# Performance work log

Measured on AMD Instinct MI355X. Metric: run time of the kernel, lower is better.

## Reference

```python
import jax, jax.numpy as jnp
import numpy as np

DIM = 1024
N_HEADS = 16
D_K = DIM // N_HEADS
B, N = 2, 2048


def _pairwise_dist(p):
    # p: [B, N, 3] -> Euclidean cdist [B, N, N], grad-safe at zero distance
    sq = jnp.sum(p * p, axis=-1)                      # [B, N]
    d2 = sq[:, :, None] + sq[:, None, :] - 2.0 * jnp.einsum('bnd,bmd->bnm', p, p)
    d2 = jnp.maximum(d2, 0.0)
    safe = jnp.where(d2 > 0.0, d2, 1.0)
    return jnp.where(d2 > 0.0, jnp.sqrt(safe), 0.0)


def setup_inputs() -> dict:
    key = jax.random.key(0)
    ks = jax.random.split(key, 11)
    s = 1.0 / np.sqrt(DIM)
    inp = {
        'x': jax.random.normal(ks[0], (B, N, DIM), jnp.float32),
        'positions': jax.random.normal(ks[1], (B, N, 3), jnp.float32),
        'W_q': jax.random.normal(ks[2], (DIM, DIM), jnp.float32) * s,
        'b_q': jnp.zeros((DIM,), jnp.float32),
        'W_k': jax.random.normal(ks[3], (DIM, DIM), jnp.float32) * s,
        'b_k': jnp.zeros((DIM,), jnp.float32),
        'W_v': jax.random.normal(ks[4], (DIM, DIM), jnp.float32) * s,
        'b_v': jnp.zeros((DIM,), jnp.float32),
        'W_o': jax.random.normal(ks[5], (DIM, DIM), jnp.float32) * s,
        'b_o': jnp.zeros((DIM,), jnp.float32),
        'dist_bias': jax.random.normal(ks[6], (N_HEADS, 1, 1), jnp.float32),
    }
    return inp


def reference(x, positions, W_q, b_q, W_k, b_k, W_v, b_v, W_o, b_o, dist_bias):
    Bv, Nv, C = x.shape
    def proj(W, b):
        # [B,N,C] -> [B,H,N,d_k]
        return (x @ W.T + b).reshape(Bv, Nv, N_HEADS, D_K).transpose(0, 2, 1, 3)
    Q = proj(W_q, b_q)
    K = proj(W_k, b_k)
    V = proj(W_v, b_v)
    attn = jnp.einsum('bhnd,bhmd->bhnm', Q, K) / np.sqrt(D_K)  # [B,H,N,N]
    dists = _pairwise_dist(positions)                          # [B,N,N]
    # log(exp(-|b|*d) + 1e-8), per-head bias broadcast over [B,H,N,N]
    dist_weights = jnp.exp(-jnp.abs(dist_bias)[None] * dists[:, None])
    attn = attn + jnp.log(dist_weights + 1e-8)
    attn = jax.nn.softmax(attn, axis=-1)
    out = jnp.einsum('bhnm,bhmd->bhnd', attn, V)               # [B,H,N,d_k]
    out = out.transpose(0, 2, 1, 3).reshape(Bv, Nv, C)
    return out @ W_o.T + b_o
```

## Files before the change

kernel.cpp:

```cpp
#include <hip/hip_runtime.h>
#include <hip/hip_bf16.h>
#include <stdint.h>

using bf16   = __hip_bfloat16;
using short8 = __attribute__((ext_vector_type(8))) short;
using f32x4  = __attribute__((ext_vector_type(4))) float;
using f32x16 = __attribute__((ext_vector_type(16))) float;

#define NSEQ   2048
#define NHEADS 16
#define DK     64
#define DMODEL 1024

#define GLDS16(gp, lp) __builtin_amdgcn_global_load_lds( \
    (const __attribute__((address_space(1))) void*)(gp), \
    (__attribute__((address_space(3))) void*)(lp), 16, 0, 0)

__device__ __forceinline__ ushort f2bf(float f){
  bf16 h = __float2bfloat16(f);
  return __builtin_bit_cast(ushort, h);
}
__device__ __forceinline__ float bf2f(ushort u){
  uint t = ((uint)u)<<16; return __builtin_bit_cast(float, t);
}

__global__ void k_cvt(const float4* __restrict__ src, ushort4* __restrict__ dst, int n4){
  int i = blockIdx.x*blockDim.x + threadIdx.x;
  if (i >= n4) return;
  float4 v = src[i];
  ushort4 o;
  o.x = f2bf(v.x); o.y = f2bf(v.y); o.z = f2bf(v.z); o.w = f2bf(v.w);
  dst[i] = o;
}

__global__ void k_geo(const float* __restrict__ pos, ushort* __restrict__ AF,
                      ushort* __restrict__ BF, int n){
  int i = blockIdx.x*blockDim.x + threadIdx.x;
  if (i >= n) return;
  float x = pos[i*3+0], y = pos[i*3+1], z = pos[i*3+2];
  float sq = x*x + y*y + z*z;
  ushort xh = f2bf(x);  float xhf = bf2f(xh);  ushort xl = f2bf(x - xhf);
  ushort yh = f2bf(y);  float yhf = bf2f(yh);  ushort yl = f2bf(y - yhf);
  ushort zh = f2bf(z);  float zhf = bf2f(zh);  ushort zl = f2bf(z - zhf);
  ushort sh = f2bf(sq); float shf = bf2f(sh);  ushort sl = f2bf(sq - shf);
  ushort m2xh = f2bf(-2.f*xhf), m2xl = f2bf(-2.f*bf2f(xl));
  ushort m2yh = f2bf(-2.f*yhf), m2yl = f2bf(-2.f*bf2f(yl));
  ushort m2zh = f2bf(-2.f*zhf), m2zl = f2bf(-2.f*bf2f(zl));
  const ushort one = 0x3F80;
  ushort af[16] = {xh,xl,xh, yh,yl,yh, zh,zl,zh, sh,sl, one,one, 0,0,0};
  ushort bv[16] = {m2xh,m2xh,m2xl, m2yh,m2yh,m2yl, m2zh,m2zh,m2zl, one,one, sh,sl, 0,0,0};
  *(uint4*)&AF[i*16]     = *(uint4*)&af[0];
  *(uint4*)&AF[i*16 + 8] = *(uint4*)&af[8];
  *(uint4*)&BF[i*16]     = *(uint4*)&bv[0];
  *(uint4*)&BF[i*16 + 8] = *(uint4*)&bv[8];
}

__device__ __forceinline__ void gemm_core(
    const ushort* __restrict__ Ap, const ushort* __restrict__ Bp,
    int bm, int bn, int tid, ushort smem[2][2][4096], f32x4 (&acc)[4][4])
{
  const int wave = tid>>6, lane = tid&63;
  const int wr = wave>>1, wc = wave&1;
  const int ko   = (lane>>4)*8;
  const int srow = wave*16 + (lane>>2);
  const int scol = (lane&3)*8;

  const ushort* As = Ap + (size_t)(bm*128)*DMODEL + scol;
  const ushort* Bs = Bp + (size_t)(bn*128)*DMODEL + scol;

#define STAGEG(buf, kt) do { \
    _Pragma("unroll") \
    for (int i_=0;i_<2;i_++){ \
      GLDS16(As + (size_t)(i_*64 + srow)*DMODEL + (kt)*32, &smem[buf][0][i_*2048 + wave*512]); \
      GLDS16(Bs + (size_t)(i_*64 + srow)*DMODEL + (kt)*32, &smem[buf][1][i_*2048 + wave*512]); \
    } } while(0)

  STAGEG(0, 0);
  for (int kt=0; kt<32; ++kt){
    int cur = kt&1;
    __syncthreads();
    if (kt<31) STAGEG(cur^1, kt+1);
    short8 af[4], bfv[4];
    const ushort* At = smem[cur][0];
    const ushort* Bt = smem[cur][1];
    #pragma unroll
    for (int mi=0;mi<4;mi++) af[mi]  = *(const short8*)&At[(wr*64+mi*16+(lane&15))*32 + ko];
    #pragma unroll
    for (int ni=0;ni<4;ni++) bfv[ni] = *(const short8*)&Bt[(wc*64+ni*16+(lane&15))*32 + ko];
    #pragma unroll
    for (int mi=0;mi<4;mi++)
      #pragma unroll
      for (int ni=0;ni<4;ni++)
        acc[mi][ni] = __builtin_amdgcn_mfma_f32_16x16x32_bf16(af[mi], bfv[ni], acc[mi][ni], 0,0,0);
  }
#undef STAGEG
}

__global__ __launch_bounds__(256) void k_gemm_qkv(
    const ushort* __restrict__ xb,
    const ushort* __restrict__ Wqb, const ushort* __restrict__ Wkb, const ushort* __restrict__ Wvb,
    const float* __restrict__ bq, const float* __restrict__ bk, const float* __restrict__ bv,
    ushort* __restrict__ Qo, ushort* __restrict__ Ko, ushort* __restrict__ Vto)
{
  __shared__ ushort smem[2][2][4096];
  const int tid = threadIdx.x;
  const int t = blockIdx.x & 255;
  const int z = blockIdx.x >> 8;
  const int lane = tid&63, wave = tid>>6;
  const int wr = wave>>1, wc = wave&1;

  const ushort* Ap; const ushort* Bp; const float* bias;
  ushort* outp; int bm, bn; float scale = 1.0f;
  if (z==0){ Ap=xb;  Bp=Wqb; bias=bq; outp=Qo;  bm=t>>3; bn=t&7; scale=0.125f; }
  else if (z==1){ Ap=xb;  Bp=Wkb; bias=bk; outp=Ko;  bm=t>>3; bn=t&7; }
  else          { Ap=Wvb; Bp=xb;  bias=bv; outp=Vto; bm=t&7;  bn=t>>3; }

  f32x4 acc[4][4] = {};
  gemm_core(Ap, Bp, bm, bn, tid, smem, acc);

  if (z<2){
    #pragma unroll
    for (int mi=0;mi<4;mi++){
      const int m0 = bm*128 + wr*64 + mi*16 + (lane>>4)*4;
      #pragma unroll
      for (int ni=0;ni<4;ni++){
        const int nn = bn*128 + wc*64 + ni*16 + (lane&15);
        const float bs = bias[nn];
        const int h = nn>>6, d = nn&63;
        #pragma unroll
        for (int j=0;j<4;j++){
          int mm = m0+j;
          int b = mm>>11, nr = mm&2047;
          size_t off = (((size_t)(b*NHEADS+h)*NSEQ) + nr)*DK + d;
          outp[off] = f2bf((acc[mi][ni][j] + bs)*scale);
        }
      }
    }
  } else {
    #pragma unroll
    for (int mi=0;mi<4;mi++){
      const int m0 = bm*128 + wr*64 + mi*16 + (lane>>4)*4;
      #pragma unroll
      for (int ni=0;ni<4;ni++){
        const int nn = bn*128 + wc*64 + ni*16 + (lane&15);
        const int b = nn>>11, nr = nn&2047;
        #pragma unroll
        for (int j=0;j<4;j++){
          int mm = m0+j;
          const float bs = bias[mm];
          int h = mm>>6, d = mm&63;
          size_t off = (((size_t)(b*NHEADS+h)*DK) + d)*NSEQ + nr;
          outp[off] = f2bf(acc[mi][ni][j] + bs);
        }
      }
    }
  }
}

__global__ __launch_bounds__(256) void k_gemm_out(
    const ushort* __restrict__ Ob, const ushort* __restrict__ Wob,
    const float* __restrict__ bo, float* __restrict__ out)
{
  __shared__ ushort smem[2][2][4096];
  const int tid = threadIdx.x;
  const int t = blockIdx.x;
  const int lane = tid&63, wave = tid>>6;
  const int wr = wave>>1, wc = wave&1;
  const int bm = t>>3, bn = t&7;
  f32x4 acc[4][4] = {};
  gemm_core(Ob, Wob, bm, bn, tid, smem, acc);
  #pragma unroll
  for (int mi=0;mi<4;mi++){
    const int m0 = bm*128 + wr*64 + mi*16 + (lane>>4)*4;
    #pragma unroll
    for (int ni=0;ni<4;ni++){
      const int nn = bn*128 + wc*64 + ni*16 + (lane&15);
      const float bs = bo[nn];
      #pragma unroll
      for (int j=0;j<4;j++)
        out[(size_t)(m0+j)*DMODEL + nn] = acc[mi][ni][j] + bs;
    }
  }
}

__global__ __launch_bounds__(256) void k_attn(
    const ushort* __restrict__ Q, const ushort* __restrict__ K, const ushort* __restrict__ Vt,
    const ushort* __restrict__ AF, const ushort* __restrict__ BF,
    const float* __restrict__ dist_bias,
    ushort* __restrict__ O)
{
  __shared__ ushort kb[2][4096];
  __shared__ ushort vb[2][4096];
  const int tid = threadIdx.x, wave = tid>>6, lane = tid&63;
  const int qt = blockIdx.x, h = blockIdx.y, b = blockIdx.z;
  const int lo5 = lane&31, hi = lane>>5;
  const float ah = fabsf(dist_bias[h]);
  const ushort* Qh  = Q  + ((size_t)(b*NHEADS+h))*NSEQ*DK;
  const ushort* Kh  = K  + ((size_t)(b*NHEADS+h))*NSEQ*DK;
  const ushort* Vth = Vt + ((size_t)(b*NHEADS+h))*DK*NSEQ;
  const ushort* AFb = AF + (size_t)b*NSEQ*16;
  const ushort* BFb = BF + (size_t)b*NSEQ*16;

  const int q0 = qt*128 + wave*32;

  short8 qf[4];
  #pragma unroll
  for (int s=0;s<4;s++)
    qf[s] = *(const short8*)&Qh[(size_t)(q0+lo5)*DK + s*16 + hi*8];
  const short8 bfq = *(const short8*)&BFb[(size_t)(q0+lo5)*16 + hi*8];

  const int grow  = lane>>3;
  const int gc16  = (lane&7) ^ grow;
  const int rowb  = wave*8 + grow;

#define STAGE(buf, jb) do { \
    _Pragma("unroll") \
    for (int p_=0;p_<2;p_++){ \
      const int rw_ = p_*32 + rowb; \
      GLDS16(Kh  + (size_t)((jb)+rw_)*DK   + gc16*8, &kb[buf][(p_*256 + wave*64)*8]); \
      GLDS16(Vth + (size_t)rw_*NSEQ + (jb) + gc16*8, &vb[buf][(p_*256 + wave*64)*8]); \
    } } while(0)

  const int rb = lo5*64;
  const int rx = lo5 & 7;

  f32x16 o0 = {}, o1 = {};
  float l_run = 0.f;

  STAGE(0, 0);
  for (int t=0; t<32; ++t){
    const int cur = t&1;
    __syncthreads();
    if (t<31) STAGE(cur^1, (t+1)*64);
    const ushort* kbc = kb[cur];
    const ushort* vbc = vb[cur];
    #pragma unroll
    for (int ss=0; ss<2; ++ss){
      const int jb = t*64 + ss*32;
      const short8 afk = *(const short8*)&AFb[(size_t)(jb+lo5)*16 + hi*8];
      f32x16 zz = {};
      f32x16 d2 = __builtin_amdgcn_mfma_f32_32x32x16_bf16(afk, bfq, zz, 0,0,0);
      const short8 kf0 = *(const short8*)&kbc[ss*2048 + rb + (((0+hi)^rx)<<3)];
      const short8 kf1 = *(const short8*)&kbc[ss*2048 + rb + (((2+hi)^rx)<<3)];
      const short8 kf2 = *(const short8*)&kbc[ss*2048 + rb + (((4+hi)^rx)<<3)];
      const short8 kf3 = *(const short8*)&kbc[ss*2048 + rb + (((6+hi)^rx)<<3)];
      f32x16 st = {};
      st = __builtin_amdgcn_mfma_f32_32x32x16_bf16(kf0, qf[0], st, 0,0,0);
      st = __builtin_amdgcn_mfma_f32_32x32x16_bf16(kf1, qf[1], st, 0,0,0);
      st = __builtin_amdgcn_mfma_f32_32x32x16_bf16(kf2, qf[2], st, 0,0,0);
      st = __builtin_amdgcn_mfma_f32_32x32x16_bf16(kf3, qf[3], st, 0,0,0);
      float p[16];
      #pragma unroll
      for (int r=0;r<16;r++){
        float d = __builtin_amdgcn_sqrtf(fmaxf(d2[r], 0.f));
        p[r] = __expf(fmaf(-ah, d, st[r]));
      }
      float s01=p[0]+p[1], s23=p[2]+p[3], s45=p[4]+p[5], s67=p[6]+p[7];
      float s89=p[8]+p[9], sab=p[10]+p[11], scd=p[12]+p[13], sef=p[14]+p[15];
      float rsum = ((s01+s23)+(s45+s67)) + ((s89+sab)+(scd+sef));
      rsum += __shfl_xor(rsum, 32);
      l_run += rsum;
      #pragma unroll
      for (int s=0;s<2;s++){
        uint w0, w1, w2, w3;
        asm("v_cvt_pk_bf16_f32 %0, %1, %2" : "=v"(w0) : "v"(p[8*s+0]), "v"(p[8*s+1]));
        asm("v_cvt_pk_bf16_f32 %0, %1, %2" : "=v"(w2) : "v"(p[8*s+4]), "v"(p[8*s+5]));
        asm("v_cvt_pk_bf16_f32 %0, %1, %2" : "=v"(w1) : "v"(p[8*s+2]), "v"(p[8*s+3]));
        asm("v_cvt_pk_bf16_f32 %0, %1, %2" : "=v"(w3) : "v"(p[8*s+6]), "v"(p[8*s+7]));
        asm volatile("v_permlane32_swap_b32 %0, %1" : "+v"(w0), "+v"(w2));
        asm volatile("v_permlane32_swap_b32 %0, %1" : "+v"(w1), "+v"(w3));
        uint4 aw; aw.x = w0; aw.y = w1; aw.z = w2; aw.w = w3;
        const short8 pa = __builtin_bit_cast(short8, aw);
        const int jcol = (ss<<2) + 2*s + hi;
        const short8 v0 = *(const short8*)&vbc[       rb + ((jcol^rx)<<3)];
        const short8 v1 = *(const short8*)&vbc[2048 + rb + ((jcol^rx)<<3)];
        o0 = __builtin_amdgcn_mfma_f32_32x32x16_bf16(pa, v0, o0, 0,0,0);
        o1 = __builtin_amdgcn_mfma_f32_32x32x16_bf16(pa, v1, o1, 0,0,0);
      }
    }
  }
#undef STAGE

  #pragma unroll
  for (int r=0;r<16;r++){
    const int src = (r&3) + 8*(r>>2) + 4*hi;
    const float lr = __shfl(l_run, src);
    const float inv = 1.f/lr;
    const int i = q0 + src;
    O[((size_t)b*NSEQ + i)*DMODEL + h*DK + lo5]      = f2bf(o0[r]*inv);
    O[((size_t)b*NSEQ + i)*DMODEL + h*DK + 32 + lo5] = f2bf(o1[r]*inv);
  }
}

extern "C" void kernel_launch(void* const* d_in, const int* in_sizes, int n_in,
                              void* d_out, int out_size, void* d_ws, size_t ws_size,
                              hipStream_t stream) {
  const float* x   = (const float*)d_in[0];
  const float* pos = (const float*)d_in[1];
  const float* Wq  = (const float*)d_in[2];
  const float* bq  = (const float*)d_in[3];
  const float* Wk  = (const float*)d_in[4];
  const float* bk  = (const float*)d_in[5];
  const float* Wv  = (const float*)d_in[6];
  const float* bv  = (const float*)d_in[7];
  const float* Wo  = (const float*)d_in[8];
  const float* bo  = (const float*)d_in[9];
  const float* db  = (const float*)d_in[10];
  float* out = (float*)d_out;

  char* ws = (char*)d_ws;
  ushort* xb   = (ushort*)(ws);
  ushort* Wqb  = (ushort*)(ws + ((size_t)8<<20));
  ushort* Wkb  = (ushort*)(ws + ((size_t)10<<20));
  ushort* Wvb  = (ushort*)(ws + ((size_t)12<<20));
  ushort* Wob  = (ushort*)(ws + ((size_t)14<<20));
  ushort* Qb   = (ushort*)(ws + ((size_t)16<<20));
  ushort* Kb   = (ushort*)(ws + ((size_t)24<<20));
  ushort* Vtb  = (ushort*)(ws + ((size_t)32<<20));
  ushort* AFt  = Wqb;
  ushort* BFt  = (ushort*)(ws + ((size_t)8<<20) + (128<<10));
  ushort* Omrg = xb;

  k_cvt<<<4096, 256, 0, stream>>>((const float4*)x,  (ushort4*)xb,  1048576);
  k_cvt<<<1024, 256, 0, stream>>>((const float4*)Wq, (ushort4*)Wqb, 262144);
  k_cvt<<<1024, 256, 0, stream>>>((const float4*)Wk, (ushort4*)Wkb, 262144);
  k_cvt<<<1024, 256, 0, stream>>>((const float4*)Wv, (ushort4*)Wvb, 262144);
  k_cvt<<<1024, 256, 0, stream>>>((const float4*)Wo, (ushort4*)Wob, 262144);
  k_gemm_qkv<<<768, 256, 0, stream>>>(xb, Wqb, Wkb, Wvb, bq, bk, bv, Qb, Kb, Vtb);
  k_geo<<<16, 256, 0, stream>>>(pos, AFt, BFt, 2*NSEQ);
  k_attn<<<dim3(16,NHEADS,2), 256, 0, stream>>>(Qb, Kb, Vtb, AFt, BFt, db, Omrg);
  k_gemm_out<<<256, 256, 0, stream>>>(Omrg, Wob, bo, out);
}
```

Measured before the change: 237.1 us.

## Merge conversion kernels, remap block indices per XCD, use exp2 softmax

Replaces five fp32-to-bf16 conversion launches with one combined kernel to cut launch overhead. Remaps block indices in the QKV, output and attention kernels so work sharing operands lands on the same XCD (blockIdx mod 8), aiming for better L2 reuse. Folds log2(e) into the Q scale and the distance coefficient so the softmax uses exp2 instead of exp, saving a multiply per element. The remapping assumes round-robin dispatch of blocks across the 8 XCDs.

```diff
diff --git a/kernel.cpp b/kernel.cpp
--- a/kernel.cpp
+++ b/kernel.cpp
@@ -11,6 +11,7 @@
 #define NHEADS 16
 #define DK     64
 #define DMODEL 1024
+#define LOG2E  1.44269504088896f
 
 #define GLDS16(gp, lp) __builtin_amdgcn_global_load_lds( \
     (const __attribute__((address_space(1))) void*)(gp), \
@@ -24,13 +25,30 @@
   uint t = ((uint)u)<<16; return __builtin_bit_cast(float, t);
 }
 
-__global__ void k_cvt(const float4* __restrict__ src, ushort4* __restrict__ dst, int n4){
-  int i = blockIdx.x*blockDim.x + threadIdx.x;
-  if (i >= n4) return;
-  float4 v = src[i];
+__global__ void k_cvt_all(const float4* __restrict__ x,  const float4* __restrict__ wq,
+                          const float4* __restrict__ wk, const float4* __restrict__ wv,
+                          const float4* __restrict__ wo,
+                          ushort4* __restrict__ xb,  ushort4* __restrict__ wqb,
+                          ushort4* __restrict__ wkb, ushort4* __restrict__ wvb,
+                          ushort4* __restrict__ wob){
+  const int i = blockIdx.x*blockDim.x + threadIdx.x;
+  const float4* s; ushort4* d; int off;
+  if (i < 1048576){ s = x; d = xb; off = i; }
+  else {
+    const int wi = i - 1048576;
+    const int w  = wi >> 18;
+    off = wi & 262143;
+    switch(w){
+      case 0:  s = wq; d = wqb; break;
+      case 1:  s = wk; d = wkb; break;
+      case 2:  s = wv; d = wvb; break;
+      default: s = wo; d = wob; break;
+    }
+  }
+  float4 v = s[off];
   ushort4 o;
   o.x = f2bf(v.x); o.y = f2bf(v.y); o.z = f2bf(v.z); o.w = f2bf(v.w);
-  dst[i] = o;
+  d[off] = o;
 }
 
 __global__ void k_geo(const float* __restrict__ pos, ushort* __restrict__ AF,
@@ -104,14 +122,15 @@
 {
   __shared__ ushort smem[2][2][4096];
   const int tid = threadIdx.x;
-  const int t = blockIdx.x & 255;
-  const int z = blockIdx.x >> 8;
+  const int work = (blockIdx.x & 7)*96 + (blockIdx.x >> 3);
+  const int t = work & 255;
+  const int z = work >> 8;
   const int lane = tid&63, wave = tid>>6;
   const int wr = wave>>1, wc = wave&1;
 
   const ushort* Ap; const ushort* Bp; const float* bias;
   ushort* outp; int bm, bn; float scale = 1.0f;
-  if (z==0){ Ap=xb;  Bp=Wqb; bias=bq; outp=Qo;  bm=t>>3; bn=t&7; scale=0.125f; }
+  if (z==0){ Ap=xb;  Bp=Wqb; bias=bq; outp=Qo;  bm=t>>3; bn=t&7; scale=0.125f*LOG2E; }
   else if (z==1){ Ap=xb;  Bp=Wkb; bias=bk; outp=Ko;  bm=t>>3; bn=t&7; }
   else          { Ap=Wvb; Bp=xb;  bias=bv; outp=Vto; bm=t&7;  bn=t>>3; }
 
@@ -163,10 +182,10 @@
 {
   __shared__ ushort smem[2][2][4096];
   const int tid = threadIdx.x;
-  const int t = blockIdx.x;
+  const int work = (blockIdx.x & 7)*32 + (blockIdx.x >> 3);
   const int lane = tid&63, wave = tid>>6;
   const int wr = wave>>1, wc = wave&1;
-  const int bm = t>>3, bn = t&7;
+  const int bm = work>>3, bn = work&7;
   f32x4 acc[4][4] = {};
   gemm_core(Ob, Wob, bm, bn, tid, smem, acc);
   #pragma unroll
@@ -192,9 +211,10 @@
   __shared__ ushort kb[2][4096];
   __shared__ ushort vb[2][4096];
   const int tid = threadIdx.x, wave = tid>>6, lane = tid&63;
-  const int qt = blockIdx.x, h = blockIdx.y, b = blockIdx.z;
+  const int work = ((blockIdx.x & 7) << 6) | (blockIdx.x >> 3);
+  const int qt = work & 15, h = (work >> 4) & 15, b = work >> 8;
   const int lo5 = lane&31, hi = lane>>5;
-  const float ah = fabsf(dist_bias[h]);
+  const float ah2 = fabsf(dist_bias[h]) * LOG2E;
   const ushort* Qh  = Q  + ((size_t)(b*NHEADS+h))*NSEQ*DK;
   const ushort* Kh  = K  + ((size_t)(b*NHEADS+h))*NSEQ*DK;
   const ushort* Vth = Vt + ((size_t)(b*NHEADS+h))*DK*NSEQ;
@@ -253,7 +273,7 @@
       #pragma unroll
       for (int r=0;r<16;r++){
         float d = __builtin_amdgcn_sqrtf(fmaxf(d2[r], 0.f));
-        p[r] = __expf(fmaf(-ah, d, st[r]));
+        p[r] = __builtin_exp2f(fmaf(-ah2, d, st[r]));
       }
       float s01=p[0]+p[1], s23=p[2]+p[3], s45=p[4]+p[5], s67=p[6]+p[7];
       float s89=p[8]+p[9], sab=p[10]+p[11], scd=p[12]+p[13], sef=p[14]+p[15];
@@ -321,13 +341,11 @@
   ushort* BFt  = (ushort*)(ws + ((size_t)8<<20) + (128<<10));
   ushort* Omrg = xb;
 
-  k_cvt<<<4096, 256, 0, stream>>>((const float4*)x,  (ushort4*)xb,  1048576);
-  k_cvt<<<1024, 256, 0, stream>>>((const float4*)Wq, (ushort4*)Wqb, 262144);
-  k_cvt<<<1024, 256, 0, stream>>>((const float4*)Wk, (ushort4*)Wkb, 262144);
-  k_cvt<<<1024, 256, 0, stream>>>((const float4*)Wv, (ushort4*)Wvb, 262144);
-  k_cvt<<<1024, 256, 0, stream>>>((const float4*)Wo, (ushort4*)Wob, 262144);
+  k_cvt_all<<<10240, 256, 0, stream>>>(
+      (const float4*)x, (const float4*)Wq, (const float4*)Wk, (const float4*)Wv, (const float4*)Wo,
+      (ushort4*)xb, (ushort4*)Wqb, (ushort4*)Wkb, (ushort4*)Wvb, (ushort4*)Wob);
   k_gemm_qkv<<<768, 256, 0, stream>>>(xb, Wqb, Wkb, Wvb, bq, bk, bv, Qb, Kb, Vtb);
   k_geo<<<16, 256, 0, stream>>>(pos, AFt, BFt, 2*NSEQ);
-  k_attn<<<dim3(16,NHEADS,2), 256, 0, stream>>>(Qb, Kb, Vtb, AFt, BFt, db, Omrg);
+  k_attn<<<512, 256, 0, stream>>>(Qb, Kb, Vtb, AFt, BFt, db, Omrg);
   k_gemm_out<<<256, 256, 0, stream>>>(Omrg, Wob, bo, out);
 }
```

After: 243.5 us. 1.03x slower.
